# Performance work log

Hardware: AMD Instinct MI355X
Metric: run time of the kernel (lower is better)

Reference implementation:

```python
import jax, jax.numpy as jnp
import numpy as np

N = 131072
N_DIM = 128
NUM_LAYERS = 8
N_MID = NUM_LAYERS - 2  # middle (n_dim -> n_dim) layers


def _sigmoid_layer(h, u_un, w_un, log_a, b):
    # h: [N, in]; u_un: [out, in]; w_un: [out, out]; log_a, b: [out, 1]
    a = jnp.exp(log_a)                      # [out, 1]
    u = jax.nn.softmax(u_un, axis=1)        # row-softmax, matches Softmax(dim=1)
    w = jax.nn.softmax(w_un, axis=1)
    inner = h @ (a * u).T + b[:, 0]         # [N, out]
    return jax.nn.sigmoid(inner) @ w.T      # [N, out]


def setup_inputs() -> dict:
    key = jax.random.key(0)
    ks = jax.random.split(key, 24)
    d = N_DIM
    inp = {
        "x": jax.random.normal(ks[0], (N,), jnp.float32),
        "fy0": jax.random.normal(ks[1], (N,), jnp.float32),
        # first layer (in=2, out=d)
        "u0": jax.random.normal(ks[2], (d, 2), jnp.float32),
        "w0": jax.random.normal(ks[3], (d, d), jnp.float32),
        "la0": jax.random.normal(ks[4], (d, 1), jnp.float32),
        "b0": jax.random.normal(ks[5], (d, 1), jnp.float32),
        # middle layers stacked (in=d, out=d)
        "uM": jax.random.normal(ks[6], (N_MID, d, d), jnp.float32),
        "wM": jax.random.normal(ks[7], (N_MID, d, d), jnp.float32),
        "laM": jax.random.normal(ks[8], (N_MID, d, 1), jnp.float32),
        "bM": jax.random.normal(ks[9], (N_MID, d, 1), jnp.float32),
        # last layer (in=d, out=1)
        "uL": jax.random.normal(ks[10], (1, d), jnp.float32),
        "wL": jax.random.normal(ks[11], (1, 1), jnp.float32),
        "laL": jax.random.normal(ks[12], (1, 1), jnp.float32),
        "bL": jax.random.normal(ks[13], (1, 1), jnp.float32),
        # MLP 1 -> 50 -> 50 -> 1
        "W1": jax.random.normal(ks[14], (50, 1), jnp.float32) * 0.2,
        "b1": jax.random.normal(ks[15], (50,), jnp.float32) * 0.2,
        "W2": jax.random.normal(ks[16], (50, 50), jnp.float32) * 0.1,
        "b2": jax.random.normal(ks[17], (50,), jnp.float32) * 0.1,
        "W3": jax.random.normal(ks[18], (1, 50), jnp.float32) * 0.1,
        "b3": jax.random.normal(ks[19], (1,), jnp.float32) * 0.1,
    }
    return inp


def reference(x, fy0, u0, w0, la0, b0, uM, wM, laM, bM, uL, wL, laL, bL,
              W1, b1, W2, b2, W3, b3):
    # MLP feature net on fy0: [N,1] -> [N,1]
    h = jax.nn.relu(fy0[:, None] @ W1.T + b1)
    h = jax.nn.relu(h @ W2.T + b2)
    theta = h @ W3.T + b3                          # [N, 1]
    mono = jnp.concatenate([x[:, None], theta], 1)  # [N, 2]

    mono = _sigmoid_layer(mono, u0, w0, la0, b0)    # [N, d]

    def step(carry, p):
        u_un, w_un, log_a, b = p
        return _sigmoid_layer(carry, u_un, w_un, log_a, b), None

    mono, _ = jax.lax.scan(step, mono, (uM, wM, laM, bM))
    out = _sigmoid_layer(mono, uL, wL, laL, bL)     # [N, 1]
    return out[:, :, None]                          # [N, 1, 1] matches torch
```

## Files before the change

### kernel.cpp

```cpp
#include <hip/hip_runtime.h>
#include <cstdint>

typedef __attribute__((ext_vector_type(8))) _Float16 half8;
typedef __attribute__((ext_vector_type(2))) _Float16 half2v;
typedef __attribute__((ext_vector_type(16))) float f32x16;
typedef __attribute__((ext_vector_type(4))) float f4;

#define LOG2E 1.44269504088896340f
#define KNL  (-1.44269504088896340f)

__device__ __forceinline__ float fast_exp(float x) { return __builtin_amdgcn_exp2f(LOG2E * x); }
__device__ __forceinline__ float sigmoidf(float v) {
    return __builtin_amdgcn_rcpf(1.f + __builtin_amdgcn_exp2f(KNL * v));
}
__device__ __forceinline__ float sigx(float v, float nb) {
    return __builtin_amdgcn_rcpf(1.f + __builtin_amdgcn_exp2f(fmaf(v, KNL, nb)));
}
__device__ __forceinline__ unsigned pk2(float a, float b) {
    half2v h = { (_Float16)a, (_Float16)b };
    return __builtin_bit_cast(unsigned, h);
}
__device__ __forceinline__ void swapl(unsigned& a, unsigned& b) {
    asm volatile("v_permlane32_swap_b32 %0, %1" : "+v"(a), "+v"(b));
}
__device__ __forceinline__ void swaplf(float& a, float& b) {
    asm volatile("v_permlane32_swap_b32 %0, %1" : "+v"(a), "+v"(b));
}
union BU { unsigned u[4]; half8 h; };

constexpr int A0X = 0, A0T = 128, B0O = 256, BMO = 384, VLO = 1152,
              W1P = 1280, B1P = 1344, B2P = 1408, W3P = 1472, CN = 1536;

constexpr int GOFF  = 0;
constexpr int W2HI  = 6 * 65536;
constexpr int W2LO  = W2HI + 8192;
constexpr int CGOFF = W2LO + 8192;

__global__ __launch_bounds__(256)
void prep_kernel(const float* __restrict__ u0, const float* __restrict__ w0,
                 const float* __restrict__ la0, const float* __restrict__ b0,
                 const float* __restrict__ uM, const float* __restrict__ wM,
                 const float* __restrict__ laM, const float* __restrict__ bM,
                 const float* __restrict__ uL, const float* __restrict__ laL,
                 const float* __restrict__ W1, const float* __restrict__ b1,
                 const float* __restrict__ W2, const float* __restrict__ b2,
                 const float* __restrict__ W3,
                 char* __restrict__ G, _Float16* __restrict__ W2hi,
                 _Float16* __restrict__ W2lo, float* __restrict__ CgF)
{
    __shared__ float Wl[128 * 136];
    __shared__ float Al[32 * 132];
    __shared__ float uls[128];

    const int tid = threadIdx.x, b = blockIdx.x;
    const bool mblk = (b < 24);
    const int l = mblk ? (b >> 2) : 6;

    {
        const float* Wsrc = (l == 0) ? w0 : wM + (l - 1) * 16384;
        const int r = tid >> 1, h = tid & 1;
        const float* rp = Wsrc + r * 128 + h * 64;
        f4 buf[16];
#pragma unroll
        for (int v = 0; v < 16; ++v) buf[v] = *(const f4*)(rp + 4 * v);
        float mx = -1e30f;
#pragma unroll
        for (int v = 0; v < 16; ++v)
#pragma unroll
            for (int e = 0; e < 4; ++e) mx = fmaxf(mx, buf[v][e]);
        mx = fmaxf(mx, __shfl_xor(mx, 1));
        float s = 0.f;
#pragma unroll
        for (int v = 0; v < 16; ++v)
#pragma unroll
            for (int e = 0; e < 4; ++e) { buf[v][e] = fast_exp(buf[v][e] - mx); s += buf[v][e]; }
        s += __shfl_xor(s, 1);
        float inv = 1.f / s;
#pragma unroll
        for (int v = 0; v < 16; ++v)
            *(f4*)(&Wl[r * 136 + h * 64 + 4 * v]) = buf[v] * inv;
    }

    if (mblk) {
        const int q = b & 3;
        const int rl = tid >> 3, part = tid & 7;
        const int gi = q * 32 + rl;
        {
            const float* up = uM + (l * 128 + gi) * 128 + part * 16;
            f4 ub[4];
#pragma unroll
            for (int v = 0; v < 4; ++v) ub[v] = *(const f4*)(up + 4 * v);
            float mx = -1e30f;
#pragma unroll
            for (int v = 0; v < 4; ++v)
#pragma unroll
                for (int e = 0; e < 4; ++e) mx = fmaxf(mx, ub[v][e]);
#pragma unroll
            for (int o = 1; o < 8; o <<= 1) mx = fmaxf(mx, __shfl_xor(mx, o));
            float s = 0.f;
#pragma unroll
            for (int v = 0; v < 4; ++v)
#pragma unroll
                for (int e = 0; e < 4; ++e) { ub[v][e] = fast_exp(ub[v][e] - mx); s += ub[v][e]; }
#pragma unroll
            for (int o = 1; o < 8; o <<= 1) s += __shfl_xor(s, o);
            float sc = fast_exp(laM[l * 128 + gi]) / s;
#pragma unroll
            for (int v = 0; v < 4; ++v)
                *(f4*)(&Al[rl * 132 + part * 16 + 4 * v]) = ub[v] * sc;
        }
        __syncthreads();
        const int j0 = (tid & 7) * 4;
        f4 acc[4] = {};
        for (int k = 0; k < 128; ++k) {
            float a = Al[rl * 132 + k];
#pragma unroll
            for (int g = 0; g < 4; ++g)
                acc[g] += a * *(const f4*)(&Wl[k * 136 + j0 + 32 * g]);
        }
        char* basehi = G + l * 65536 + gi * 256;
        char* baselo = basehi + 32768;
        const int sw = (gi & 7) << 4;
#pragma unroll
        for (int g = 0; g < 4; ++g)
#pragma unroll
            for (int e = 0; e < 4; ++e) {
                const int j = j0 + 32 * g + e;
                float m = acc[g][e];
                _Float16 hh = (_Float16)m;
                *(_Float16*)(basehi + ((2 * j) ^ sw)) = hh;
                *(_Float16*)(baselo + ((2 * j) ^ sw)) = (_Float16)(m - (float)hh);
            }
    } else {
        if (tid < 64) {
            float v0 = uL[tid], v1 = uL[tid + 64];
            float mx = fmaxf(v0, v1);
#pragma unroll
            for (int o = 32; o; o >>= 1) mx = fmaxf(mx, __shfl_xor(mx, o));
            float e0 = fast_exp(v0 - mx), e1 = fast_exp(v1 - mx);
            float ssum = e0 + e1;
#pragma unroll
            for (int o = 32; o; o >>= 1) ssum += __shfl_xor(ssum, o);
            float aL = fast_exp(laL[0]) / ssum;
            uls[tid]      = e0 * aL;
            uls[tid + 64] = e1 * aL;
        }
        __syncthreads();
        if (tid < 128) {
            float s = 0.f;
            for (int k = 0; k < 128; ++k) s += uls[k] * Wl[k * 136 + tid];
            CgF[VLO + tid] = s;
        }
        if (tid < 128) {
            const int j = tid;
            float q0 = u0[2 * j], q1 = u0[2 * j + 1];
            float mx = fmaxf(q0, q1);
            float e0 = fast_exp(q0 - mx), e1 = fast_exp(q1 - mx);
            float a = fast_exp(la0[j]) / (e0 + e1);
            CgF[A0X + j] = a * e0;
            CgF[A0T + j] = a * e1;
            CgF[B0O + j] = b0[j];
        } else if (tid < 192) {
            const int t = tid - 128;
            CgF[W1P + t] = (t < 50) ? W1[t] : 0.f;
            CgF[B1P + t] = (t < 50) ? b1[t] : 0.f;
            CgF[B2P + t] = (t < 50) ? b2[t] : 0.f;
            CgF[W3P + t] = (t < 50) ? W3[t] : 0.f;
        }
        for (int i = tid; i < 768; i += 256) CgF[BMO + i] = KNL * bM[i];
        for (int i = tid; i < 4096; i += 256) {
            int r = i >> 6, c = i & 63;
            float v = (r < 50 && c < 50) ? W2[r * 50 + c] : 0.f;
            _Float16 h = (_Float16)v;
            W2hi[i] = h;
            W2lo[i] = (_Float16)(v - (float)h);
        }
    }
}


__device__ __forceinline__ void stage64(char* ls, const char* gs, int tid) {
#pragma unroll
    for (int i = 0; i < 8; ++i)
        __builtin_amdgcn_global_load_lds(
            (const __attribute__((address_space(1))) unsigned*)(uintptr_t)(gs + tid * 16 + i * 8192),
            (__attribute__((address_space(3))) unsigned*)(uintptr_t)(ls + tid * 16 + i * 8192),
            16, 0, 0);
}

__device__ __forceinline__ void epi_nt(const f32x16& a0, const f32x16& a1,
                                       half8& o00, half8& o01, half8& o10, half8& o11,
                                       const float* __restrict__ biasNT, int hi)
{
    f4 bv0 = *(const f4*)(biasNT + 4 * hi);
    f4 bv1 = *(const f4*)(biasNT + 8 + 4 * hi);
    f4 bv2 = *(const f4*)(biasNT + 16 + 4 * hi);
    f4 bv3 = *(const f4*)(biasNT + 24 + 4 * hi);
#pragma unroll
    for (int bt = 0; bt < 2; ++bt) {
        const f32x16& A = bt ? a1 : a0;
        unsigned p00 = pk2(sigx(A[0], bv0[0]),  sigx(A[1], bv0[1]));
        unsigned p01 = pk2(sigx(A[2], bv0[2]),  sigx(A[3], bv0[3]));
        unsigned p10 = pk2(sigx(A[4], bv1[0]),  sigx(A[5], bv1[1]));
        unsigned p11 = pk2(sigx(A[6], bv1[2]),  sigx(A[7], bv1[3]));
        unsigned p20 = pk2(sigx(A[8], bv2[0]),  sigx(A[9], bv2[1]));
        unsigned p21 = pk2(sigx(A[10], bv2[2]), sigx(A[11], bv2[3]));
        unsigned p30 = pk2(sigx(A[12], bv3[0]), sigx(A[13], bv3[1]));
        unsigned p31 = pk2(sigx(A[14], bv3[2]), sigx(A[15], bv3[3]));
        swapl(p00, p10); swapl(p01, p11);
        swapl(p20, p30); swapl(p21, p31);
        BU u0; u0.u[0] = p00; u0.u[1] = p01; u0.u[2] = p10; u0.u[3] = p11;
        BU u1; u1.u[0] = p20; u1.u[1] = p21; u1.u[2] = p30; u1.u[3] = p31;
        if (bt == 0) { o00 = u0.h; o01 = u1.h; }
        else         { o10 = u0.h; o11 = u1.h; }
    }
}

__device__ __forceinline__ void do_layer(const char* buf,
                                         const half8 (&Bin)[2][8], half8 (&Bout)[2][8],
                                         const float* __restrict__ biasL,
                                         int l31, int hi)
{
    const int sw = (l31 & 7) << 4;
#pragma unroll
    for (int nt = 0; nt < 4; ++nt) {
        f32x16 a0 = {}, a1 = {};
        const char* rhi = buf + (nt * 32 + l31) * 256;
        const char* rlo = rhi + 32768;
#pragma unroll
        for (int ks = 0; ks < 8; ++ks) {
            const int off = (ks * 32 + hi * 16) ^ sw;
            half8 Ah = *(const half8*)(rhi + off);
            half8 Al = *(const half8*)(rlo + off);
            a0 = __builtin_amdgcn_mfma_f32_32x32x16_f16(Ah, Bin[0][ks], a0, 0, 0, 0);
            a1 = __builtin_amdgcn_mfma_f32_32x32x16_f16(Ah, Bin[1][ks], a1, 0, 0, 0);
            a0 = __builtin_amdgcn_mfma_f32_32x32x16_f16(Al, Bin[0][ks], a0, 0, 0, 0);
            a1 = __builtin_amdgcn_mfma_f32_32x32x16_f16(Al, Bin[1][ks], a1, 0, 0, 0);
        }
        epi_nt(a0, a1, Bout[0][2 * nt], Bout[0][2 * nt + 1],
               Bout[1][2 * nt], Bout[1][2 * nt + 1], biasL + 32 * nt, hi);
    }
}

__global__ __launch_bounds__(512, 2)
void mono_main(const float* __restrict__ x, const float* __restrict__ fy0,
               const char* __restrict__ G,
               const _Float16* __restrict__ W2hi, const _Float16* __restrict__ W2lo,
               const float* __restrict__ CgF, const float* __restrict__ b3g,
               const float* __restrict__ bLg, float* __restrict__ out)
{
    extern __shared__ __align__(16) char sm[];
    char* buf0 = sm;
    char* buf1 = sm + 65536;

    const int tid = threadIdx.x;
    const int lane = tid & 63, wave = tid >> 6;
    const int l31 = lane & 31, hi = lane >> 5;
    const int row0 = blockIdx.x * 512 + wave * 64;

    stage64(buf0, G, tid);
    const float b3s = b3g[0], bLs = bLg[0];

    float fy[2] = { fy0[row0 + l31], fy0[row0 + 32 + l31] };
    half8 Bm[2][4];
#pragma unroll
    for (int ks = 0; ks < 4; ++ks) {
        f4 w1a = *(const f4*)(CgF + W1P + 16 * ks + 8 * hi);
        f4 w1b = *(const f4*)(CgF + W1P + 16 * ks + 8 * hi + 4);
        f4 b1a = *(const f4*)(CgF + B1P + 16 * ks + 8 * hi);
        f4 b1b = *(const f4*)(CgF + B1P + 16 * ks + 8 * hi + 4);
#pragma unroll
        for (int bt = 0; bt < 2; ++bt) {
            BU u;
            u.u[0] = pk2(fmaxf(fy[bt] * w1a[0] + b1a[0], 0.f), fmaxf(fy[bt] * w1a[1] + b1a[1], 0.f));
            u.u[1] = pk2(fmaxf(fy[bt] * w1a[2] + b1a[2], 0.f), fmaxf(fy[bt] * w1a[3] + b1a[3], 0.f));
            u.u[2] = pk2(fmaxf(fy[bt] * w1b[0] + b1b[0], 0.f), fmaxf(fy[bt] * w1b[1] + b1b[1], 0.f));
            u.u[3] = pk2(fmaxf(fy[bt] * w1b[2] + b1b[2], 0.f), fmaxf(fy[bt] * w1b[3] + b1b[3], 0.f));
            Bm[bt][ks] = u.h;
        }
    }

    f32x16 a00 = {}, a01 = {}, a10 = {}, a11 = {};
#pragma unroll
    for (int nt = 0; nt < 2; ++nt)
#pragma unroll
        for (int ks = 0; ks < 4; ++ks) {
            half8 Ah = *(const half8*)(W2hi + (nt * 32 + l31) * 64 + ks * 16 + hi * 8);
            half8 Al = *(const half8*)(W2lo + (nt * 32 + l31) * 64 + ks * 16 + hi * 8);
            if (nt == 0) {
                a00 = __builtin_amdgcn_mfma_f32_32x32x16_f16(Ah, Bm[0][ks], a00, 0, 0, 0);
                a10 = __builtin_amdgcn_mfma_f32_32x32x16_f16(Ah, Bm[1][ks], a10, 0, 0, 0);
                a00 = __builtin_amdgcn_mfma_f32_32x32x16_f16(Al, Bm[0][ks], a00, 0, 0, 0);
                a10 = __builtin_amdgcn_mfma_f32_32x32x16_f16(Al, Bm[1][ks], a10, 0, 0, 0);
            } else {
                a01 = __builtin_amdgcn_mfma_f32_32x32x16_f16(Ah, Bm[0][ks], a01, 0, 0, 0);
                a11 = __builtin_amdgcn_mfma_f32_32x32x16_f16(Ah, Bm[1][ks], a11, 0, 0, 0);
                a01 = __builtin_amdgcn_mfma_f32_32x32x16_f16(Al, Bm[0][ks], a01, 0, 0, 0);
                a11 = __builtin_amdgcn_mfma_f32_32x32x16_f16(Al, Bm[1][ks], a11, 0, 0, 0);
            }
        }

    float tp0 = 0.f, tp1 = 0.f;
#pragma unroll
    for (int nt = 0; nt < 2; ++nt)
#pragma unroll
        for (int g = 0; g < 4; ++g) {
            f4 w3 = *(const f4*)(CgF + W3P + 32 * nt + 8 * g + 4 * hi);
            f4 b2v = *(const f4*)(CgF + B2P + 32 * nt + 8 * g + 4 * hi);
            const f32x16& A0 = nt ? a01 : a00;
            const f32x16& A1 = nt ? a11 : a10;
#pragma unroll
            for (int e = 0; e < 4; ++e) {
                tp0 += w3[e] * fmaxf(A0[4 * g + e] + b2v[e], 0.f);
                tp1 += w3[e] * fmaxf(A1[4 * g + e] + b2v[e], 0.f);
            }
        }
    swaplf(tp0, tp1);
    float th = tp0 + tp1 + b3s;
    float t0 = th, t1 = th;
    swaplf(t0, t1);

    float xr[2] = { x[row0 + l31], x[row0 + 32 + l31] };
    float thv[2] = { t0, t1 };
    half8 Bq[2][8], Bp[2][8];
#pragma unroll
    for (int ks = 0; ks < 8; ++ks) {
        f4 axa = *(const f4*)(CgF + A0X + 16 * ks + 8 * hi);
        f4 axb = *(const f4*)(CgF + A0X + 16 * ks + 8 * hi + 4);
        f4 ata = *(const f4*)(CgF + A0T + 16 * ks + 8 * hi);
        f4 atb = *(const f4*)(CgF + A0T + 16 * ks + 8 * hi + 4);
        f4 b0a = *(const f4*)(CgF + B0O + 16 * ks + 8 * hi);
        f4 b0b = *(const f4*)(CgF + B0O + 16 * ks + 8 * hi + 4);
#pragma unroll
        for (int bt = 0; bt < 2; ++bt) {
            BU u;
            u.u[0] = pk2(sigmoidf(axa[0] * xr[bt] + ata[0] * thv[bt] + b0a[0]),
                         sigmoidf(axa[1] * xr[bt] + ata[1] * thv[bt] + b0a[1]));
            u.u[1] = pk2(sigmoidf(axa[2] * xr[bt] + ata[2] * thv[bt] + b0a[2]),
                         sigmoidf(axa[3] * xr[bt] + ata[3] * thv[bt] + b0a[3]));
            u.u[2] = pk2(sigmoidf(axb[0] * xr[bt] + atb[0] * thv[bt] + b0b[0]),
                         sigmoidf(axb[1] * xr[bt] + atb[1] * thv[bt] + b0b[1]));
            u.u[3] = pk2(sigmoidf(axb[2] * xr[bt] + atb[2] * thv[bt] + b0b[2]),
                         sigmoidf(axb[3] * xr[bt] + atb[3] * thv[bt] + b0b[3]));
            Bq[bt][ks] = u.h;
        }
    }
    __syncthreads();

    stage64(buf1, G + 1 * 65536, tid);
    do_layer(buf0, Bq, Bp, CgF + BMO + 0 * 128, l31, hi);
    __syncthreads();
    stage64(buf0, G + 2 * 65536, tid);
    do_layer(buf1, Bp, Bq, CgF + BMO + 1 * 128, l31, hi);
    __syncthreads();
    stage64(buf1, G + 3 * 65536, tid);
    do_layer(buf0, Bq, Bp, CgF + BMO + 2 * 128, l31, hi);
    __syncthreads();
    stage64(buf0, G + 4 * 65536, tid);
    do_layer(buf1, Bp, Bq, CgF + BMO + 3 * 128, l31, hi);
    __syncthreads();
    stage64(buf1, G + 5 * 65536, tid);
    do_layer(buf0, Bq, Bp, CgF + BMO + 4 * 128, l31, hi);
    __syncthreads();
    do_layer(buf1, Bp, Bq, CgF + BMO + 5 * 128, l31, hi);

    float d0 = 0.f, d1 = 0.f;
#pragma unroll
    for (int ks = 0; ks < 8; ++ks) {
        f4 va = *(const f4*)(CgF + VLO + 16 * ks + 8 * hi);
        f4 vb = *(const f4*)(CgF + VLO + 16 * ks + 8 * hi + 4);
        half8 s0 = Bq[0][ks], s1 = Bq[1][ks];
#pragma unroll
        for (int e = 0; e < 4; ++e) {
            d0 += va[e] * (float)s0[e] + vb[e] * (float)s0[e + 4];
            d1 += va[e] * (float)s1[e] + vb[e] * (float)s1[e + 4];
        }
    }
    swaplf(d0, d1);
    out[row0 + lane] = sigmoidf(d0 + d1 + bLs);
}

extern "C" void kernel_launch(void* const* d_in, const int* in_sizes, int n_in,
                              void* d_out, int out_size, void* d_ws, size_t ws_size,
                              hipStream_t stream)
{
    const float* x   = (const float*)d_in[0];
    const float* fy0 = (const float*)d_in[1];
    const float* u0  = (const float*)d_in[2];
    const float* w0  = (const float*)d_in[3];
    const float* la0 = (const float*)d_in[4];
    const float* b0  = (const float*)d_in[5];
    const float* uM  = (const float*)d_in[6];
    const float* wM  = (const float*)d_in[7];
    const float* laM = (const float*)d_in[8];
    const float* bM  = (const float*)d_in[9];
    const float* uL  = (const float*)d_in[10];
    const float* laL = (const float*)d_in[12];
    const float* bL  = (const float*)d_in[13];
    const float* W1  = (const float*)d_in[14];
    const float* b1  = (const float*)d_in[15];
    const float* W2  = (const float*)d_in[16];
    const float* b2  = (const float*)d_in[17];
    const float* W3  = (const float*)d_in[18];
    const float* b3  = (const float*)d_in[19];
    float* out = (float*)d_out;

    char* ws = (char*)d_ws;
    char*     Gz   = ws + GOFF;
    _Float16* W2hi = (_Float16*)(ws + W2HI);
    _Float16* W2lo = (_Float16*)(ws + W2LO);
    float*    CgF  = (float*)(ws + CGOFF);

    prep_kernel<<<25, 256, 0, stream>>>(u0, w0, la0, b0, uM, wM, laM, bM,
                                        uL, laL, W1, b1, W2, b2, W3,
                                        Gz, W2hi, W2lo, CgF);

    static bool attr_set = false;
    if (!attr_set) {
        hipFuncSetAttribute((const void*)mono_main,
                            hipFuncAttributeMaxDynamicSharedMemorySize, 131072);
        attr_set = true;
    }
    mono_main<<<256, 512, 131072, stream>>>(x, fy0, Gz, W2hi, W2lo, CgF, b3, bL, out);
}
```

Baseline: 154.6 us.

## Stage only hi weight halves in LDS, read lo halves from global, fold bias

Splits the per-layer fp16 weights into separate hi and lo arrays. Only the hi half is double-buffered into LDS, and the lo correction terms are read straight from global/L2 inside the MFMA loop. This halves LDS use, which allows 512 blocks of 256 threads at two blocks per CU instead of 256 blocks of 512. The -log2e scale and the bias are folded into the prepared weights and into the MFMA accumulator initialisation, so the epilogue no longer does an fma per element. Prep is spread over 96 blocks instead of 24. The risk is extra global-load latency on the lo path inside the inner loop.

```diff
diff --git a/kernel.cpp b/kernel.cpp
--- a/kernel.cpp
+++ b/kernel.cpp
@@ -2,6 +2,7 @@
 #include <cstdint>
 
 typedef __attribute__((ext_vector_type(8))) _Float16 half8;
+typedef __attribute__((ext_vector_type(4))) _Float16 half4;
 typedef __attribute__((ext_vector_type(2))) _Float16 half2v;
 typedef __attribute__((ext_vector_type(16))) float f32x16;
 typedef __attribute__((ext_vector_type(4))) float f4;
@@ -13,8 +14,8 @@
 __device__ __forceinline__ float sigmoidf(float v) {
     return __builtin_amdgcn_rcpf(1.f + __builtin_amdgcn_exp2f(KNL * v));
 }
-__device__ __forceinline__ float sigx(float v, float nb) {
-    return __builtin_amdgcn_rcpf(1.f + __builtin_amdgcn_exp2f(fmaf(v, KNL, nb)));
+__device__ __forceinline__ float sig2(float y) {
+    return __builtin_amdgcn_rcpf(1.f + __builtin_amdgcn_exp2f(y));
 }
 __device__ __forceinline__ unsigned pk2(float a, float b) {
     half2v h = { (_Float16)a, (_Float16)b };
@@ -31,10 +32,11 @@
 constexpr int A0X = 0, A0T = 128, B0O = 256, BMO = 384, VLO = 1152,
               W1P = 1280, B1P = 1344, B2P = 1408, W3P = 1472, CN = 1536;
 
-constexpr int GOFF  = 0;
-constexpr int W2HI  = 6 * 65536;
-constexpr int W2LO  = W2HI + 8192;
-constexpr int CGOFF = W2LO + 8192;
+constexpr int GHIO  = 0;
+constexpr int GLOO  = 6 * 32768;
+constexpr int W2HIO = 12 * 32768;
+constexpr int W2LOO = W2HIO + 8192;
+constexpr int CGOFF = W2LOO + 8192;
 
 __global__ __launch_bounds__(256)
 void prep_kernel(const float* __restrict__ u0, const float* __restrict__ w0,
@@ -45,16 +47,17 @@
                  const float* __restrict__ W1, const float* __restrict__ b1,
                  const float* __restrict__ W2, const float* __restrict__ b2,
                  const float* __restrict__ W3,
-                 char* __restrict__ G, _Float16* __restrict__ W2hi,
-                 _Float16* __restrict__ W2lo, float* __restrict__ CgF)
+                 char* __restrict__ Ghi, char* __restrict__ Glo,
+                 _Float16* __restrict__ W2hi, _Float16* __restrict__ W2lo,
+                 float* __restrict__ CgF)
 {
     __shared__ float Wl[128 * 136];
-    __shared__ float Al[32 * 132];
+    __shared__ float Al[8 * 132];
     __shared__ float uls[128];
 
     const int tid = threadIdx.x, b = blockIdx.x;
-    const bool mblk = (b < 24);
-    const int l = mblk ? (b >> 2) : 6;
+    const bool mblk = (b < 96);
+    const int l = mblk ? (b >> 4) : 6;
 
     {
         const float* Wsrc = (l == 0) ? w0 : wM + (l - 1) * 16384;
@@ -82,55 +85,42 @@
     }
 
     if (mblk) {
-        const int q = b & 3;
-        const int rl = tid >> 3, part = tid & 7;
-        const int gi = q * 32 + rl;
+        const int q = b & 15;
+        const int rl = tid >> 5, part = tid & 31;
+        const int gi = q * 8 + rl;
         {
-            const float* up = uM + (l * 128 + gi) * 128 + part * 16;
-            f4 ub[4];
-#pragma unroll
-            for (int v = 0; v < 4; ++v) ub[v] = *(const f4*)(up + 4 * v);
-            float mx = -1e30f;
-#pragma unroll
-            for (int v = 0; v < 4; ++v)
-#pragma unroll
-                for (int e = 0; e < 4; ++e) mx = fmaxf(mx, ub[v][e]);
-#pragma unroll
-            for (int o = 1; o < 8; o <<= 1) mx = fmaxf(mx, __shfl_xor(mx, o));
+            f4 ub = *(const f4*)(uM + (l * 128 + gi) * 128 + part * 4);
+            float mx = fmaxf(fmaxf(ub[0], ub[1]), fmaxf(ub[2], ub[3]));
+#pragma unroll
+            for (int o = 1; o < 32; o <<= 1) mx = fmaxf(mx, __shfl_xor(mx, o));
             float s = 0.f;
 #pragma unroll
-            for (int v = 0; v < 4; ++v)
-#pragma unroll
-                for (int e = 0; e < 4; ++e) { ub[v][e] = fast_exp(ub[v][e] - mx); s += ub[v][e]; }
-#pragma unroll
-            for (int o = 1; o < 8; o <<= 1) s += __shfl_xor(s, o);
+            for (int e = 0; e < 4; ++e) { ub[e] = fast_exp(ub[e] - mx); s += ub[e]; }
+#pragma unroll
+            for (int o = 1; o < 32; o <<= 1) s += __shfl_xor(s, o);
             float sc = fast_exp(laM[l * 128 + gi]) / s;
-#pragma unroll
-            for (int v = 0; v < 4; ++v)
-                *(f4*)(&Al[rl * 132 + part * 16 + 4 * v]) = ub[v] * sc;
+            *(f4*)(&Al[rl * 132 + part * 4]) = ub * sc;
         }
         __syncthreads();
-        const int j0 = (tid & 7) * 4;
-        f4 acc[4] = {};
+        const int j0 = part * 4;
+        f4 acc = {};
         for (int k = 0; k < 128; ++k) {
             float a = Al[rl * 132 + k];
-#pragma unroll
-            for (int g = 0; g < 4; ++g)
-                acc[g] += a * *(const f4*)(&Wl[k * 136 + j0 + 32 * g]);
-        }
-        char* basehi = G + l * 65536 + gi * 256;
-        char* baselo = basehi + 32768;
-        const int sw = (gi & 7) << 4;
-#pragma unroll
-        for (int g = 0; g < 4; ++g)
-#pragma unroll
-            for (int e = 0; e < 4; ++e) {
-                const int j = j0 + 32 * g + e;
-                float m = acc[g][e];
-                _Float16 hh = (_Float16)m;
-                *(_Float16*)(basehi + ((2 * j) ^ sw)) = hh;
-                *(_Float16*)(baselo + ((2 * j) ^ sw)) = (_Float16)(m - (float)hh);
-            }
+            acc += a * *(const f4*)(&Wl[k * 136 + j0]);
+        }
+        const int sw = (gi & 15) << 4;
+        char* bh = Ghi + l * 32768 + gi * 256;
+        char* bl = Glo + l * 32768 + gi * 256;
+        half4 hv, lv;
+#pragma unroll
+        for (int e = 0; e < 4; ++e) {
+            float m = KNL * acc[e];
+            _Float16 hh = (_Float16)m;
+            hv[e] = hh;
+            lv[e] = (_Float16)(m - (float)hh);
+        }
+        *(half4*)(bh + ((2 * j0) ^ sw)) = hv;
+        *(half4*)(bl + 2 * j0) = lv;
     } else {
         if (tid < 64) {
             float v0 = uL[tid], v1 = uL[tid + 64];
@@ -157,9 +147,9 @@
             float mx = fmaxf(q0, q1);
             float e0 = fast_exp(q0 - mx), e1 = fast_exp(q1 - mx);
             float a = fast_exp(la0[j]) / (e0 + e1);
-            CgF[A0X + j] = a * e0;
-            CgF[A0T + j] = a * e1;
-            CgF[B0O + j] = b0[j];
+            CgF[A0X + j] = KNL * a * e0;
+            CgF[A0T + j] = KNL * a * e1;
+            CgF[B0O + j] = KNL * b0[j];
         } else if (tid < 192) {
             const int t = tid - 128;
             CgF[W1P + t] = (t < 50) ? W1[t] : 0.f;
@@ -179,34 +169,29 @@
 }
 
 
-__device__ __forceinline__ void stage64(char* ls, const char* gs, int tid) {
+__device__ __forceinline__ void stage32(char* ls, const char* gs, int tid) {
 #pragma unroll
     for (int i = 0; i < 8; ++i)
         __builtin_amdgcn_global_load_lds(
-            (const __attribute__((address_space(1))) unsigned*)(uintptr_t)(gs + tid * 16 + i * 8192),
-            (__attribute__((address_space(3))) unsigned*)(uintptr_t)(ls + tid * 16 + i * 8192),
+            (const __attribute__((address_space(1))) unsigned*)(uintptr_t)(gs + tid * 16 + i * 4096),
+            (__attribute__((address_space(3))) unsigned*)(uintptr_t)(ls + tid * 16 + i * 4096),
             16, 0, 0);
 }
 
 __device__ __forceinline__ void epi_nt(const f32x16& a0, const f32x16& a1,
-                                       half8& o00, half8& o01, half8& o10, half8& o11,
-                                       const float* __restrict__ biasNT, int hi)
+                                       half8& o00, half8& o01, half8& o10, half8& o11)
 {
-    f4 bv0 = *(const f4*)(biasNT + 4 * hi);
-    f4 bv1 = *(const f4*)(biasNT + 8 + 4 * hi);
-    f4 bv2 = *(const f4*)(biasNT + 16 + 4 * hi);
-    f4 bv3 = *(const f4*)(biasNT + 24 + 4 * hi);
 #pragma unroll
     for (int bt = 0; bt < 2; ++bt) {
         const f32x16& A = bt ? a1 : a0;
-        unsigned p00 = pk2(sigx(A[0], bv0[0]),  sigx(A[1], bv0[1]));
-        unsigned p01 = pk2(sigx(A[2], bv0[2]),  sigx(A[3], bv0[3]));
-        unsigned p10 = pk2(sigx(A[4], bv1[0]),  sigx(A[5], bv1[1]));
-        unsigned p11 = pk2(sigx(A[6], bv1[2]),  sigx(A[7], bv1[3]));
-        unsigned p20 = pk2(sigx(A[8], bv2[0]),  sigx(A[9], bv2[1]));
-        unsigned p21 = pk2(sigx(A[10], bv2[2]), sigx(A[11], bv2[3]));
-        unsigned p30 = pk2(sigx(A[12], bv3[0]), sigx(A[13], bv3[1]));
-        unsigned p31 = pk2(sigx(A[14], bv3[2]), sigx(A[15], bv3[3]));
+        unsigned p00 = pk2(sig2(A[0]),  sig2(A[1]));
+        unsigned p01 = pk2(sig2(A[2]),  sig2(A[3]));
+        unsigned p10 = pk2(sig2(A[4]),  sig2(A[5]));
+        unsigned p11 = pk2(sig2(A[6]),  sig2(A[7]));
+        unsigned p20 = pk2(sig2(A[8]),  sig2(A[9]));
+        unsigned p21 = pk2(sig2(A[10]), sig2(A[11]));
+        unsigned p30 = pk2(sig2(A[12]), sig2(A[13]));
+        unsigned p31 = pk2(sig2(A[14]), sig2(A[15]));
         swapl(p00, p10); swapl(p01, p11);
         swapl(p20, p30); swapl(p21, p31);
         BU u0; u0.u[0] = p00; u0.u[1] = p01; u0.u[2] = p10; u0.u[3] = p11;
@@ -216,49 +201,56 @@
     }
 }
 
-__device__ __forceinline__ void do_layer(const char* buf,
+__device__ __forceinline__ void do_layer(const char* bufHi, const char* gLo,
                                          const half8 (&Bin)[2][8], half8 (&Bout)[2][8],
-                                         const float* __restrict__ biasL,
+                                         const float* __restrict__ biasK,
                                          int l31, int hi)
 {
-    const int sw = (l31 & 7) << 4;
+    const int sw = (l31 & 15) << 4;
 #pragma unroll
     for (int nt = 0; nt < 4; ++nt) {
-        f32x16 a0 = {}, a1 = {};
-        const char* rhi = buf + (nt * 32 + l31) * 256;
-        const char* rlo = rhi + 32768;
+        f4 bv0 = *(const f4*)(biasK + 32 * nt + 4 * hi);
+        f4 bv1 = *(const f4*)(biasK + 32 * nt + 8 + 4 * hi);
+        f4 bv2 = *(const f4*)(biasK + 32 * nt + 16 + 4 * hi);
+        f4 bv3 = *(const f4*)(biasK + 32 * nt + 24 + 4 * hi);
+        f32x16 a0 = { bv0[0], bv0[1], bv0[2], bv0[3],
+                      bv1[0], bv1[1], bv1[2], bv1[3],
+                      bv2[0], bv2[1], bv2[2], bv2[3],
+                      bv3[0], bv3[1], bv3[2], bv3[3] };
+        f32x16 a1 = a0;
+        const char* rhi = bufHi + (nt * 32 + l31) * 256;
+        const char* rlo = gLo + (nt * 32 + l31) * 256;
 #pragma unroll
         for (int ks = 0; ks < 8; ++ks) {
-            const int off = (ks * 32 + hi * 16) ^ sw;
-            half8 Ah = *(const half8*)(rhi + off);
-            half8 Al = *(const half8*)(rlo + off);
+            half8 Ah = *(const half8*)(rhi + ((ks * 32 + hi * 16) ^ sw));
+            half8 Al = *(const half8*)(rlo + ks * 32 + hi * 16);
             a0 = __builtin_amdgcn_mfma_f32_32x32x16_f16(Ah, Bin[0][ks], a0, 0, 0, 0);
             a1 = __builtin_amdgcn_mfma_f32_32x32x16_f16(Ah, Bin[1][ks], a1, 0, 0, 0);
             a0 = __builtin_amdgcn_mfma_f32_32x32x16_f16(Al, Bin[0][ks], a0, 0, 0, 0);
             a1 = __builtin_amdgcn_mfma_f32_32x32x16_f16(Al, Bin[1][ks], a1, 0, 0, 0);
         }
         epi_nt(a0, a1, Bout[0][2 * nt], Bout[0][2 * nt + 1],
-               Bout[1][2 * nt], Bout[1][2 * nt + 1], biasL + 32 * nt, hi);
-    }
-}
-
-__global__ __launch_bounds__(512, 2)
+               Bout[1][2 * nt], Bout[1][2 * nt + 1]);
+    }
+}
+
+__global__ __launch_bounds__(256, 2)
 void mono_main(const float* __restrict__ x, const float* __restrict__ fy0,
-               const char* __restrict__ G,
+               const char* __restrict__ Ghi, const char* __restrict__ Glo,
                const _Float16* __restrict__ W2hi, const _Float16* __restrict__ W2lo,
                const float* __restrict__ CgF, const float* __restrict__ b3g,
                const float* __restrict__ bLg, float* __restrict__ out)
 {
     extern __shared__ __align__(16) char sm[];
     char* buf0 = sm;
-    char* buf1 = sm + 65536;
+    char* buf1 = sm + 32768;
 
     const int tid = threadIdx.x;
     const int lane = tid & 63, wave = tid >> 6;
     const int l31 = lane & 31, hi = lane >> 5;
-    const int row0 = blockIdx.x * 512 + wave * 64;
-
-    stage64(buf0, G, tid);
+    const int row0 = blockIdx.x * 256 + wave * 64;
+
+    stage32(buf0, Ghi, tid);
     const float b3s = b3g[0], bLs = bLg[0];
 
     float fy[2] = { fy0[row0 + l31], fy0[row0 + 32 + l31] };
@@ -334,35 +326,35 @@
 #pragma unroll
         for (int bt = 0; bt < 2; ++bt) {
             BU u;
-            u.u[0] = pk2(sigmoidf(axa[0] * xr[bt] + ata[0] * thv[bt] + b0a[0]),
-                         sigmoidf(axa[1] * xr[bt] + ata[1] * thv[bt] + b0a[1]));
-            u.u[1] = pk2(sigmoidf(axa[2] * xr[bt] + ata[2] * thv[bt] + b0a[2]),
-                         sigmoidf(axa[3] * xr[bt] + ata[3] * thv[bt] + b0a[3]));
-            u.u[2] = pk2(sigmoidf(axb[0] * xr[bt] + atb[0] * thv[bt] + b0b[0]),
-                         sigmoidf(axb[1] * xr[bt] + atb[1] * thv[bt] + b0b[1]));
-            u.u[3] = pk2(sigmoidf(axb[2] * xr[bt] + atb[2] * thv[bt] + b0b[2]),
-                         sigmoidf(axb[3] * xr[bt] + atb[3] * thv[bt] + b0b[3]));
+            u.u[0] = pk2(sig2(axa[0] * xr[bt] + ata[0] * thv[bt] + b0a[0]),
+                         sig2(axa[1] * xr[bt] + ata[1] * thv[bt] + b0a[1]));
+            u.u[1] = pk2(sig2(axa[2] * xr[bt] + ata[2] * thv[bt] + b0a[2]),
+                         sig2(axa[3] * xr[bt] + ata[3] * thv[bt] + b0a[3]));
+            u.u[2] = pk2(sig2(axb[0] * xr[bt] + atb[0] * thv[bt] + b0b[0]),
+                         sig2(axb[1] * xr[bt] + atb[1] * thv[bt] + b0b[1]));
+            u.u[3] = pk2(sig2(axb[2] * xr[bt] + atb[2] * thv[bt] + b0b[2]),
+                         sig2(axb[3] * xr[bt] + atb[3] * thv[bt] + b0b[3]));
             Bq[bt][ks] = u.h;
         }
     }
     __syncthreads();
 
-    stage64(buf1, G + 1 * 65536, tid);
-    do_layer(buf0, Bq, Bp, CgF + BMO + 0 * 128, l31, hi);
-    __syncthreads();
-    stage64(buf0, G + 2 * 65536, tid);
-    do_layer(buf1, Bp, Bq, CgF + BMO + 1 * 128, l31, hi);
-    __syncthreads();
-    stage64(buf1, G + 3 * 65536, tid);
-    do_layer(buf0, Bq, Bp, CgF + BMO + 2 * 128, l31, hi);
-    __syncthreads();
-    stage64(buf0, G + 4 * 65536, tid);
-    do_layer(buf1, Bp, Bq, CgF + BMO + 3 * 128, l31, hi);
-    __syncthreads();
-    stage64(buf1, G + 5 * 65536, tid);
-    do_layer(buf0, Bq, Bp, CgF + BMO + 4 * 128, l31, hi);
-    __syncthreads();
-    do_layer(buf1, Bp, Bq, CgF + BMO + 5 * 128, l31, hi);
+    stage32(buf1, Ghi + 1 * 32768, tid);
+    do_layer(buf0, Glo + 0 * 32768, Bq, Bp, CgF + BMO + 0 * 128, l31, hi);
+    __syncthreads();
+    stage32(buf0, Ghi + 2 * 32768, tid);
+    do_layer(buf1, Glo + 1 * 32768, Bp, Bq, CgF + BMO + 1 * 128, l31, hi);
+    __syncthreads();
+    stage32(buf1, Ghi + 3 * 32768, tid);
+    do_layer(buf0, Glo + 2 * 32768, Bq, Bp, CgF + BMO + 2 * 128, l31, hi);
+    __syncthreads();
+    stage32(buf0, Ghi + 4 * 32768, tid);
+    do_layer(buf1, Glo + 3 * 32768, Bp, Bq, CgF + BMO + 3 * 128, l31, hi);
+    __syncthreads();
+    stage32(buf1, Ghi + 5 * 32768, tid);
+    do_layer(buf0, Glo + 4 * 32768, Bq, Bp, CgF + BMO + 4 * 128, l31, hi);
+    __syncthreads();
+    do_layer(buf1, Glo + 5 * 32768, Bp, Bq, CgF + BMO + 5 * 128, l31, hi);
 
     float d0 = 0.f, d1 = 0.f;
 #pragma unroll
@@ -406,20 +398,22 @@
     float* out = (float*)d_out;
 
     char* ws = (char*)d_ws;
-    char*     Gz   = ws + GOFF;
-    _Float16* W2hi = (_Float16*)(ws + W2HI);
-    _Float16* W2lo = (_Float16*)(ws + W2LO);
+    char*     Ghi  = ws + GHIO;
+    char*     Glo  = ws + GLOO;
+    _Float16* W2hi = (_Float16*)(ws + W2HIO);
+    _Float16* W2lo = (_Float16*)(ws + W2LOO);
     float*    CgF  = (float*)(ws + CGOFF);
 
-    prep_kernel<<<25, 256, 0, stream>>>(u0, w0, la0, b0, uM, wM, laM, bM,
+    prep_kernel<<<97, 256, 0, stream>>>(u0, w0, la0, b0, uM, wM, laM, bM,
                                         uL, laL, W1, b1, W2, b2, W3,
-                                        Gz, W2hi, W2lo, CgF);
+                                        Ghi, Glo, W2hi, W2lo, CgF);
 
     static bool attr_set = false;
     if (!attr_set) {
         hipFuncSetAttribute((const void*)mono_main,
-                            hipFuncAttributeMaxDynamicSharedMemorySize, 131072);
+                            hipFuncAttributeMaxDynamicSharedMemorySize, 65536);
         attr_set = true;
     }
-    mono_main<<<256, 512, 131072, stream>>>(x, fy0, Gz, W2hi, W2lo, CgF, b3, bL, out);
-}
+    mono_main<<<512, 256, 65536, stream>>>(x, fy0, Ghi, Glo, W2hi, W2lo,
+                                           CgF, b3, bL, out);
+}
```

After: 169.0 us. +9.3%, slower.
